# Kernel tuning notes

Hardware: AMD Instinct MI355X
Metric: run time of the kernel (lower is better)

Reference implementation:

```python
import jax, jax.numpy as jnp
import numpy as np
from jax import lax

BIG = 1e6  # sentinel 1D distance when no zero seen yet (squared stays finite in fp32)


def edt_2d(binary):
    """Exact Euclidean distance transform of a (B, H, W) binary image.

    Matches scipy.ndimage.distance_transform_edt: for each nonzero pixel,
    distance to the nearest zero pixel. Separable formulation:
      pass 1: g[b,i,c]   = min_r |i - r| s.t. binary[b,r,c] == 0   (two scans)
      pass 2: d2[b,i,j]  = min_c g[b,i,c]^2 + (j - c)^2            (broadcast-min)
    """
    B, H, W = binary.shape
    xs = jnp.moveaxis(binary, 1, 0)  # (H, B, W) -> scan over rows

    def sweep(carry, x):
        d = jnp.where(x == 0, 0.0, carry + 1.0)
        return d, d

    init = jnp.full((B, W), BIG, dtype=binary.dtype)
    _, down = lax.scan(sweep, init, xs)
    _, up = lax.scan(sweep, init, xs, reverse=True)
    g = jnp.moveaxis(jnp.minimum(down, up), 0, 1)  # (B, H, W) vertical 1D EDT

    j = jnp.arange(W, dtype=binary.dtype)
    diff2 = (j[:, None] - j[None, :]) ** 2  # (W_out, W_src)
    # (B, H, 1, W) + (W, W) -> min over source column axis
    d2 = jnp.min(g[:, :, None, :] ** 2 + diff2[None, None, :, :], axis=-1)
    return jnp.sqrt(d2)


def combo_loss(pred, target,
               dice_weight=0.5, bce_weight=0.5, boundary_weight=0.1, focal_weight=0.2,
               smooth=1.0, alpha=1.0, gamma=2.0, inner_boundary_weight=1.0):
    p = jax.nn.sigmoid(pred)

    # Dice
    intersection = jnp.sum(p * target)
    union = jnp.sum(p) + jnp.sum(target)
    dice = 1.0 - (2.0 * intersection + smooth) / (union + smooth)

    # BCEWithLogits (stable)
    bce = jnp.mean(jnp.maximum(pred, 0.0) - pred * target
                   + jnp.log1p(jnp.exp(-jnp.abs(pred))))

    # Boundary loss (torch thresholds raw pred > 0.5, detached -> stop_gradient)
    pred_bin = lax.stop_gradient((pred > 0.5).astype(pred.dtype))[:, 0]    # (B,H,W)
    targ_bin = lax.stop_gradient(target.astype(pred.dtype))[:, 0]          # (B,H,W)
    # per-sample mean then batch mean == global mean (equal-size images)
    boundary = inner_boundary_weight * jnp.mean(
        jnp.abs(edt_2d(pred_bin) - edt_2d(targ_bin)))

    # Focal
    bce_el = -(target * jnp.log(p) + (1.0 - target) * jnp.log(1.0 - p))
    pt = p * target + (1.0 - p) * (1.0 - target)
    focal = jnp.mean(alpha * (1.0 - pt) ** gamma * bce_el)

    return (dice_weight * dice + bce_weight * bce
            + boundary_weight * boundary + focal_weight * focal)


def setup_inputs() -> dict:
    key = jax.random.key(0)
    k1, k2 = jax.random.split(key)
    B, C, H, W = 4, 1, 256, 256
    pred = jax.random.normal(k1, (B, C, H, W), dtype=jnp.float32)
    target = jax.random.bernoulli(k2, 0.5, (B, C, H, W)).astype(jnp.float32)
    return {"pred": pred, "target": target}


def reference(pred, target):
    return combo_loss(pred, target)
```

## Files before the change

### kernel.cpp

```cpp
#include <hip/hip_runtime.h>
#include <math.h>

#define BB 4
#define HH 256
#define WW 256
#define NN (BB*HH*WW)
typedef unsigned long long u64;
typedef unsigned int u32;

#define MASK_OFF_BYTES 256
#define SENT 100000

__global__ __launch_bounds__(64)
void build_masks(const float* __restrict__ pred,
                 const float* __restrict__ targ,
                 float* __restrict__ ws) {
    int t = blockIdx.x * 64 + threadIdx.x;
    if (t < 7) ws[t] = 0.0f;

    int c   = t & 255;
    int h   = (t >> 8) & 1;
    int w   = (t >> 9) & 3;
    int b   = (t >> 11) & 3;
    int img = t >> 13;

    const float* s = (img ? targ : pred) + b * (HH * WW) + (w * 64 + h * 32) * WW + c;
    u32 m = 0;
    #pragma unroll
    for (int r = 0; r < 32; ++r) {
        float x = s[r * WW];
        m |= ((u32)(x <= 0.5f)) << r;
    }
    u32* mask32 = (u32*)((char*)ws + MASK_OFF_BYTES);
    mask32[(((((img * BB + b) * WW + c) << 2) + w) << 1) + h] = m;
}

__global__ __launch_bounds__(256)
void band_fused(const float* __restrict__ pred,
                const float* __restrict__ targ,
                float* __restrict__ ws,
                float* __restrict__ out) {
    __shared__ float2 G[4][WW];
    __shared__ float red[4][6];
    __shared__ int amLast;

    int blk  = blockIdx.x;
    int b    = blk >> 6;
    int band = blk & 63;
    int i0   = band << 2;
    int wq   = i0 >> 6;
    int o0   = i0 & 63;
    int c    = threadIdx.x;

    const u64* maskT = (const u64*)((const char*)ws + MASK_OFF_BYTES);

    float g2v[2][4];
    #pragma unroll
    for (int img = 0; img < 2; ++img) {
        const u64* mp = maskT + (((img * BB + b) * WW + c) << 2);
        u64 M0 = mp[0], M1 = mp[1], M2 = mp[2], M3 = mp[3];

        int t1 = __ffsll(M1), t2 = __ffsll(M2), t3 = __ffsll(M3);
        int f1 = t1 ? 64 + t1 - 1  : SENT;
        int f2 = t2 ? 128 + t2 - 1 : SENT;
        int f3 = t3 ? 192 + t3 - 1 : SENT;
        int r0 = __ffsll(__brevll(M0));
        int r1 = __ffsll(__brevll(M1));
        int r2 = __ffsll(__brevll(M2));
        int l0 = r0 ? 64 - r0  : -SENT;
        int l1 = r1 ? 128 - r1 : -SENT;
        int l2 = r2 ? 192 - r2 : -SENT;

        int s3 = f3;
        int s2 = min(f2, s3);
        int s1 = min(f1, s2);
        int NF = (wq == 0) ? s1 : (wq == 1) ? s2 : (wq == 2) ? s3 : SENT;
        int q0 = l0;
        int q1 = max(q0, l1);
        int q2 = max(q1, l2);
        int PB = (wq == 0) ? -SENT : (wq == 1) ? q0 : (wq == 2) ? q1 : q2;
        u64 Mq = (wq == 0) ? M0 : (wq == 1) ? M1 : (wq == 2) ? M2 : M3;

        #pragma unroll
        for (int kk = 0; kk < 4; ++kk) {
            int i = i0 + kk, o = o0 + kk;
            u64 sh  = Mq >> o;
            int tn  = __ffsll(sh);
            int n   = tn ? i + tn - 1 : NF;
            u64 shl = Mq << (63 - o);
            int tp  = __ffsll(__brevll(shl));
            int p   = tp ? i - (tp - 1) : PB;
            int g   = min(n - i, i - p);
            g2v[img][kk] = (float)g * (float)g;
        }
    }
    #pragma unroll
    for (int kk = 0; kk < 4; ++kk)
        G[kk][c] = make_float2(g2v[0][kk], g2v[1][kk]);
    __syncthreads();

    int j = threadIdx.x;
    float d2p[4], d2t[4];
    #pragma unroll
    for (int k = 0; k < 4; ++k) {
        float2 g = G[k][j];
        d2p[k] = g.x; d2t[k] = g.y;
    }
    for (int r = 1; r < WW; ++r) {
        float r2 = (float)(r * r);
        float dmax = fmaxf(fmaxf(fmaxf(d2p[0], d2p[1]), fmaxf(d2p[2], d2p[3])),
                           fmaxf(fmaxf(d2t[0], d2t[1]), fmaxf(d2t[2], d2t[3])));
        if (__all(r2 >= dmax)) break;
        int lo = j - r, hi = j + r;
        if (lo >= 0) {
            #pragma unroll
            for (int k = 0; k < 4; ++k) {
                float2 g = G[k][lo];
                d2p[k] = fminf(d2p[k], g.x + r2);
                d2t[k] = fminf(d2t[k], g.y + r2);
            }
        }
        if (hi < WW) {
            #pragma unroll
            for (int k = 0; k < 4; ++k) {
                float2 g = G[k][hi];
                d2p[k] = fminf(d2p[k], g.x + r2);
                d2t[k] = fminf(d2t[k], g.y + r2);
            }
        }
    }

    float sPT = 0.0f, sP = 0.0f, sT = 0.0f, sBCE = 0.0f, sFOC = 0.0f, sBND = 0.0f;
    #pragma unroll
    for (int k = 0; k < 4; ++k) {
        int idx = (b * HH + (i0 + k)) * WW + j;
        float x = pred[idx];
        float t = targ[idx];

        sBND += fabsf(sqrtf(d2p[k]) - sqrtf(d2t[k]));

        float p   = 1.0f / (1.0f + expf(-x));
        float ax  = fabsf(x);
        float l1p = log1pf(expf(-ax));
        float bce_el = fmaxf(x, 0.0f) - x * t + l1p;
        float lsx  = fminf(x, 0.0f) - l1p;
        float lsnx = -fmaxf(x, 0.0f) - l1p;
        float bce_f = -(t * lsx + (1.0f - t) * lsnx);
        float pt = p * t + (1.0f - p) * (1.0f - t);
        float om = 1.0f - pt;

        sPT  += p * t;
        sP   += p;
        sT   += t;
        sBCE += bce_el;
        sFOC += om * om * bce_f;
    }

    float vals[6] = { sPT, sP, sT, sBCE, sFOC, sBND };
    int lane = threadIdx.x & 63;
    int wave = threadIdx.x >> 6;
    #pragma unroll
    for (int k = 0; k < 6; ++k) {
        float v = vals[k];
        #pragma unroll
        for (int off = 32; off > 0; off >>= 1)
            v += __shfl_down(v, off, 64);
        if (lane == 0) red[wave][k] = v;
    }
    __syncthreads();
    if (threadIdx.x < 6) {
        float s = red[0][threadIdx.x] + red[1][threadIdx.x]
                + red[2][threadIdx.x] + red[3][threadIdx.x];
        atomicAdd(&ws[threadIdx.x], s);
        __threadfence();
    }
    __syncthreads();

    if (threadIdx.x == 0) {
        unsigned old = atomicAdd((unsigned*)(ws + 6), 1u);
        amLast = (old == 255u);
    }
    __syncthreads();
    if (amLast && threadIdx.x == 0) {
        float inter = atomicAdd(&ws[0], 0.0f);
        float sp    = atomicAdd(&ws[1], 0.0f);
        float st    = atomicAdd(&ws[2], 0.0f);
        float bce   = atomicAdd(&ws[3], 0.0f);
        float foc   = atomicAdd(&ws[4], 0.0f);
        float bnd   = atomicAdd(&ws[5], 0.0f);
        float invN = 1.0f / (float)NN;
        float dice = 1.0f - (2.0f * inter + 1.0f) / (sp + st + 1.0f);
        out[0] = 0.5f * dice + 0.5f * (bce * invN)
               + 0.1f * (bnd * invN) + 0.2f * (foc * invN);
    }
}

extern "C" void kernel_launch(void* const* d_in, const int* in_sizes, int n_in,
                              void* d_out, int out_size, void* d_ws, size_t ws_size,
                              hipStream_t stream) {
    const float* pred = (const float*)d_in[0];
    const float* targ = (const float*)d_in[1];
    float* ws = (float*)d_ws;

    build_masks<<<256, 64, 0, stream>>>(pred, targ, ws);
    band_fused<<<BB * 64, 256, 0, stream>>>(pred, targ, ws, (float*)d_out);
}
```

Baseline: 69.50 us.

## Fuse mask building into main kernel and replace atomic reduction with finalize pass

```diff
diff --git a/kernel.cpp b/kernel.cpp
--- a/kernel.cpp
+++ b/kernel.cpp
@@ -8,41 +8,16 @@
 typedef unsigned long long u64;
 typedef unsigned int u32;
 
-#define MASK_OFF_BYTES 256
 #define SENT 100000
 
-__global__ __launch_bounds__(64)
-void build_masks(const float* __restrict__ pred,
-                 const float* __restrict__ targ,
-                 float* __restrict__ ws) {
-    int t = blockIdx.x * 64 + threadIdx.x;
-    if (t < 7) ws[t] = 0.0f;
-
-    int c   = t & 255;
-    int h   = (t >> 8) & 1;
-    int w   = (t >> 9) & 3;
-    int b   = (t >> 11) & 3;
-    int img = t >> 13;
-
-    const float* s = (img ? targ : pred) + b * (HH * WW) + (w * 64 + h * 32) * WW + c;
-    u32 m = 0;
-    #pragma unroll
-    for (int r = 0; r < 32; ++r) {
-        float x = s[r * WW];
-        m |= ((u32)(x <= 0.5f)) << r;
-    }
-    u32* mask32 = (u32*)((char*)ws + MASK_OFF_BYTES);
-    mask32[(((((img * BB + b) * WW + c) << 2) + w) << 1) + h] = m;
-}
-
-__global__ __launch_bounds__(256)
-void band_fused(const float* __restrict__ pred,
+
+__global__ __launch_bounds__(512)
+void fused_main(const float* __restrict__ pred,
                 const float* __restrict__ targ,
-                float* __restrict__ ws,
-                float* __restrict__ out) {
-    __shared__ float2 G[4][WW];
-    __shared__ float red[4][6];
-    __shared__ int amLast;
+                float* __restrict__ partial) {
+    __shared__ float G[2][4][WW];
+    __shared__ float D[2][4][WW];
+    __shared__ float red[8][6];
 
     int blk  = blockIdx.x;
     int b    = blk >> 6;
@@ -50,15 +25,26 @@
     int i0   = band << 2;
     int wq   = i0 >> 6;
     int o0   = i0 & 63;
-    int c    = threadIdx.x;
-
-    const u64* maskT = (const u64*)((const char*)ws + MASK_OFF_BYTES);
-
-    float g2v[2][4];
-    #pragma unroll
-    for (int img = 0; img < 2; ++img) {
-        const u64* mp = maskT + (((img * BB + b) * WW + c) << 2);
-        u64 M0 = mp[0], M1 = mp[1], M2 = mp[2], M3 = mp[3];
+
+    int tid  = threadIdx.x;
+    int img  = tid >> 8;
+    int c    = tid & 255;
+
+    const float* s = (img ? targ : pred) + b * (HH * WW) + c;
+    u64 M[4];
+    #pragma unroll
+    for (int w = 0; w < 4; ++w) {
+        u64 m = 0;
+        #pragma unroll
+        for (int rr = 0; rr < 64; ++rr) {
+            float x = s[(w * 64 + rr) * WW];
+            m |= ((u64)(x <= 0.5f)) << rr;
+        }
+        M[w] = m;
+    }
+
+    {
+        u64 M0 = M[0], M1 = M[1], M2 = M[2], M3 = M[3];
 
         int t1 = __ffsll(M1), t2 = __ffsll(M2), t3 = __ffsll(M3);
         int f1 = t1 ? 64 + t1 - 1  : SENT;
@@ -91,53 +77,50 @@
             int tp  = __ffsll(__brevll(shl));
             int p   = tp ? i - (tp - 1) : PB;
             int g   = min(n - i, i - p);
-            g2v[img][kk] = (float)g * (float)g;
+            G[img][kk][c] = (float)g * (float)g;
         }
     }
-    #pragma unroll
-    for (int kk = 0; kk < 4; ++kk)
-        G[kk][c] = make_float2(g2v[0][kk], g2v[1][kk]);
-    __syncthreads();
-
-    int j = threadIdx.x;
-    float d2p[4], d2t[4];
-    #pragma unroll
-    for (int k = 0; k < 4; ++k) {
-        float2 g = G[k][j];
-        d2p[k] = g.x; d2t[k] = g.y;
-    }
-    for (int r = 1; r < WW; ++r) {
-        float r2 = (float)(r * r);
-        float dmax = fmaxf(fmaxf(fmaxf(d2p[0], d2p[1]), fmaxf(d2p[2], d2p[3])),
-                           fmaxf(fmaxf(d2t[0], d2t[1]), fmaxf(d2t[2], d2t[3])));
-        if (__all(r2 >= dmax)) break;
-        int lo = j - r, hi = j + r;
-        if (lo >= 0) {
-            #pragma unroll
-            for (int k = 0; k < 4; ++k) {
-                float2 g = G[k][lo];
-                d2p[k] = fminf(d2p[k], g.x + r2);
-                d2t[k] = fminf(d2t[k], g.y + r2);
+    __syncthreads();
+
+    {
+        int j = c;
+        float d2[4];
+        #pragma unroll
+        for (int k = 0; k < 4; ++k)
+            d2[k] = G[img][k][j];
+        for (int r = 1; r < WW; ++r) {
+            float r2 = (float)(r * r);
+            float dmax = fmaxf(fmaxf(d2[0], d2[1]), fmaxf(d2[2], d2[3]));
+            if (__all(r2 >= dmax)) break;
+            int lo = j - r, hi = j + r;
+            if (lo >= 0) {
+                #pragma unroll
+                for (int k = 0; k < 4; ++k)
+                    d2[k] = fminf(d2[k], G[img][k][lo] + r2);
+            }
+            if (hi < WW) {
+                #pragma unroll
+                for (int k = 0; k < 4; ++k)
+                    d2[k] = fminf(d2[k], G[img][k][hi] + r2);
             }
         }
-        if (hi < WW) {
-            #pragma unroll
-            for (int k = 0; k < 4; ++k) {
-                float2 g = G[k][hi];
-                d2p[k] = fminf(d2p[k], g.x + r2);
-                d2t[k] = fminf(d2t[k], g.y + r2);
-            }
-        }
-    }
+        #pragma unroll
+        for (int k = 0; k < 4; ++k)
+            D[img][k][j] = sqrtf(d2[k]);
+    }
+    __syncthreads();
 
     float sPT = 0.0f, sP = 0.0f, sT = 0.0f, sBCE = 0.0f, sFOC = 0.0f, sBND = 0.0f;
     #pragma unroll
-    for (int k = 0; k < 4; ++k) {
-        int idx = (b * HH + (i0 + k)) * WW + j;
+    for (int h = 0; h < 2; ++h) {
+        int q  = tid + h * 512;
+        int k  = q >> 8;
+        int j2 = q & 255;
+        int idx = (b * HH + (i0 + k)) * WW + j2;
         float x = pred[idx];
         float t = targ[idx];
 
-        sBND += fabsf(sqrtf(d2p[k]) - sqrtf(d2t[k]));
+        sBND += fabsf(D[0][k][j2] - D[1][k][j2]);
 
         float p   = 1.0f / (1.0f + expf(-x));
         float ax  = fabsf(x);
@@ -157,8 +140,8 @@
     }
 
     float vals[6] = { sPT, sP, sT, sBCE, sFOC, sBND };
-    int lane = threadIdx.x & 63;
-    int wave = threadIdx.x >> 6;
+    int lane = tid & 63;
+    int wave = tid >> 6;
     #pragma unroll
     for (int k = 0; k < 6; ++k) {
         float v = vals[k];
@@ -168,26 +151,40 @@
         if (lane == 0) red[wave][k] = v;
     }
     __syncthreads();
-    if (threadIdx.x < 6) {
-        float s = red[0][threadIdx.x] + red[1][threadIdx.x]
-                + red[2][threadIdx.x] + red[3][threadIdx.x];
-        atomicAdd(&ws[threadIdx.x], s);
-        __threadfence();
-    }
-    __syncthreads();
-
-    if (threadIdx.x == 0) {
-        unsigned old = atomicAdd((unsigned*)(ws + 6), 1u);
-        amLast = (old == 255u);
-    }
-    __syncthreads();
-    if (amLast && threadIdx.x == 0) {
-        float inter = atomicAdd(&ws[0], 0.0f);
-        float sp    = atomicAdd(&ws[1], 0.0f);
-        float st    = atomicAdd(&ws[2], 0.0f);
-        float bce   = atomicAdd(&ws[3], 0.0f);
-        float foc   = atomicAdd(&ws[4], 0.0f);
-        float bnd   = atomicAdd(&ws[5], 0.0f);
+    if (tid < 6) {
+        float s2 = 0.0f;
+        #pragma unroll
+        for (int wv = 0; wv < 8; ++wv) s2 += red[wv][tid];
+        partial[blk * 8 + tid] = s2;
+    }
+}
+
+__global__ __launch_bounds__(256)
+void finalize(const float* __restrict__ partial, float* __restrict__ out) {
+    __shared__ float red[4][6];
+    int tid = threadIdx.x;
+    float v[6];
+    #pragma unroll
+    for (int k = 0; k < 6; ++k) v[k] = partial[tid * 8 + k];
+
+    int lane = tid & 63;
+    int wave = tid >> 6;
+    #pragma unroll
+    for (int k = 0; k < 6; ++k) {
+        float x = v[k];
+        #pragma unroll
+        for (int off = 32; off > 0; off >>= 1)
+            x += __shfl_down(x, off, 64);
+        if (lane == 0) red[wave][k] = x;
+    }
+    __syncthreads();
+    if (tid == 0) {
+        float inter = red[0][0] + red[1][0] + red[2][0] + red[3][0];
+        float sp    = red[0][1] + red[1][1] + red[2][1] + red[3][1];
+        float st    = red[0][2] + red[1][2] + red[2][2] + red[3][2];
+        float bce   = red[0][3] + red[1][3] + red[2][3] + red[3][3];
+        float foc   = red[0][4] + red[1][4] + red[2][4] + red[3][4];
+        float bnd   = red[0][5] + red[1][5] + red[2][5] + red[3][5];
         float invN = 1.0f / (float)NN;
         float dice = 1.0f - (2.0f * inter + 1.0f) / (sp + st + 1.0f);
         out[0] = 0.5f * dice + 0.5f * (bce * invN)
@@ -198,10 +195,11 @@
 extern "C" void kernel_launch(void* const* d_in, const int* in_sizes, int n_in,
                               void* d_out, int out_size, void* d_ws, size_t ws_size,
                               hipStream_t stream) {
+    (void)in_sizes; (void)n_in; (void)out_size; (void)ws_size;
     const float* pred = (const float*)d_in[0];
     const float* targ = (const float*)d_in[1];
     float* ws = (float*)d_ws;
 
-    build_masks<<<256, 64, 0, stream>>>(pred, targ, ws);
-    band_fused<<<BB * 64, 256, 0, stream>>>(pred, targ, ws, (float*)d_out);
+    fused_main<<<256, 512, 0, stream>>>(pred, targ, ws);
+    finalize<<<1, 256, 0, stream>>>(ws, (float*)d_out);
 }
```

New measurement: 68.48 us (median of 2 runs). Within noise of the previous version (-1.5%).
